# Kernel optimization log

Measured on AMD Instinct MI355X. Metric: run time of the kernel, lower is better.

Reference implementation:

```python
import jax, jax.numpy as jnp
import numpy as np

N, E, H, L, G = 80000, 1280000, 64, 4, 256
ATOM_V, ATOM_F, BOND_V, BOND_F = 100, 9, 10, 3
EPS = 1e-7

def _ln(x, g, b):
    mu = jnp.mean(x, axis=-1, keepdims=True)
    var = jnp.mean((x - mu) ** 2, axis=-1, keepdims=True)
    return (x - mu) * jax.lax.rsqrt(var + 1e-5) * g + b

def setup_inputs() -> dict:
    key = jax.random.key(0)
    ks = jax.random.split(key, 16)
    inp = {}
    inp['x'] = jax.random.randint(ks[0], (N, ATOM_F), 0, ATOM_V)
    inp['edge_attr'] = jax.random.randint(ks[1], (E, BOND_F), 0, BOND_V)
    inp['edge_index'] = jax.random.randint(ks[2], (2, E), 0, N)
    inp['batch'] = jnp.sort(jax.random.randint(ks[3], (N,), 0, G))
    s = 0.05
    inp['atom_emb'] = jax.random.normal(ks[4], (ATOM_F * ATOM_V, H)) * s
    inp['bond_emb'] = jax.random.normal(ks[5], (BOND_F * BOND_V, H)) * s
    inp['t'] = jnp.ones((L,))
    inp['W1'] = jax.random.normal(ks[6], (L, H, 2 * H)) * s
    inp['b1'] = jnp.zeros((L, 2 * H))
    inp['ln1_g'] = jnp.ones((L, 2 * H))
    inp['ln1_b'] = jnp.zeros((L, 2 * H))
    inp['W2'] = jax.random.normal(ks[7], (L, 2 * H, H)) * s
    inp['b2'] = jnp.zeros((L, H))
    inp['norm_g'] = jnp.ones((L, H))
    inp['norm_b'] = jnp.zeros((L, H))
    return inp

def reference(x, edge_attr, edge_index, batch, atom_emb, bond_emb, t,
              W1, b1, ln1_g, ln1_b, W2, b2, norm_g, norm_b):
    src, dst = edge_index[0], edge_index[1]
    # encoders: sum of per-feature embeddings (flattened tables with offsets)
    xn = jnp.sum(atom_emb[x + jnp.arange(ATOM_F) * ATOM_V], axis=1)   # [N,H]
    ea = jnp.sum(bond_emb[edge_attr + jnp.arange(BOND_F) * BOND_V], axis=1)  # [E,H]

    def genconv(h, l):
        msg = jax.nn.relu(h[src] + ea) + EPS                    # [E,H]
        m = msg * t[l]
        mx = jax.ops.segment_max(m, dst, num_segments=N)        # per-dst, per-channel
        ex = jnp.exp(m - mx[dst])
        den = jax.ops.segment_sum(ex, dst, num_segments=N)
        alpha = ex / (den[dst] + 1e-16)
        agg = jax.ops.segment_sum(alpha * msg, dst, num_segments=N)
        o = agg + h                                             # root add
        mid = jax.nn.relu(_ln(o @ W1[l] + b1[l], ln1_g[l], ln1_b[l]))
        return mid @ W2[l] + b2[l]

    cur = genconv(xn, 0)
    for l in range(1, L):  # res+ blocks: x + conv(act(norm(x)))  (dropout inactive in eval)
        hh = jax.nn.relu(_ln(cur, norm_g[l], norm_b[l]))
        cur = cur + genconv(hh, l)
    out = jax.nn.relu(_ln(cur, norm_g[0], norm_b[0]))
    # per-graph mean pooling
    sums = jax.ops.segment_sum(out, batch, num_segments=G)
    cnts = jax.ops.segment_sum(jnp.ones((out.shape[0],), out.dtype), batch, num_segments=G)
    return sums / jnp.maximum(cnts, 1.0)[:, None]
```

## Files before the change

### kernel.cpp

```cpp
#include <hip/hip_runtime.h>
#include <hip/hip_bf16.h>
#include <hip/hip_fp16.h>

#define NN 80000
#define NE 1280000
#define NL 4
#define NG 256

typedef __attribute__((ext_vector_type(8))) _Float16 half8;
typedef __attribute__((ext_vector_type(4))) float f32x4;

__device__ __forceinline__ float wave_sum(float v) {
    for (int off = 32; off; off >>= 1) v += __shfl_xor(v, off, 64);
    return v;
}

__global__ void k_count(const int* __restrict__ idx, int* __restrict__ cnt) {
    int e = blockIdx.x * 256 + threadIdx.x;
    if (e < NE) atomicAdd(&cnt[idx[e]], 1);
}

__global__ void k_scan1(const int* __restrict__ in, int* __restrict__ out,
                        int* __restrict__ bsum, int n) {
    __shared__ int ws[4];
    int i = blockIdx.x * 256 + threadIdx.x;
    int v = (i < n) ? in[i] : 0;
    int lane = threadIdx.x & 63, w = threadIdx.x >> 6;
    for (int off = 1; off < 64; off <<= 1) {
        int t = __shfl_up(v, off, 64);
        if (lane >= off) v += t;
    }
    if (lane == 63) ws[w] = v;
    __syncthreads();
    if (threadIdx.x == 0) {
        int acc = 0;
        for (int k = 0; k < 4; k++) { int t = ws[k]; ws[k] = acc; acc += t; }
    }
    __syncthreads();
    v += ws[w];
    if (i < n) out[i] = v;
    if (threadIdx.x == 255) bsum[blockIdx.x] = v;
}

__global__ void k_scan2(int* __restrict__ bsum, int nb) {
    __shared__ int ws[4];
    __shared__ int carry;
    if (threadIdx.x == 0) carry = 0;
    __syncthreads();
    for (int base = 0; base < nb; base += 256) {
        int i = base + threadIdx.x;
        int v = (i < nb) ? bsum[i] : 0;
        int lane = threadIdx.x & 63, w = threadIdx.x >> 6;
        for (int off = 1; off < 64; off <<= 1) {
            int t = __shfl_up(v, off, 64);
            if (lane >= off) v += t;
        }
        if (lane == 63) ws[w] = v;
        __syncthreads();
        if (threadIdx.x == 0) {
            int acc = carry;
            for (int k = 0; k < 4; k++) { int t = ws[k]; ws[k] = acc; acc += t; }
            carry = acc;
        }
        __syncthreads();
        v += ws[w];
        if (i < nb) bsum[i] = v;
        __syncthreads();
    }
}

__global__ void k_scan3(int* __restrict__ rowptr, const int* __restrict__ bsum, int n) {
    int i = blockIdx.x * 256 + threadIdx.x;
    if (i < n) {
        int off = (blockIdx.x > 0) ? bsum[blockIdx.x - 1] : 0;
        rowptr[1 + i] += off;
    }
    if (i == 0 && blockIdx.x == 0) rowptr[0] = 0;
}

__global__ void k_fill(const int* __restrict__ src, const int* __restrict__ dst,
                       const int* __restrict__ eattr, const int* __restrict__ rowptr,
                       int* __restrict__ wofs, int* __restrict__ csr32) {
    int part = blockIdx.x & 7;
    int e = (blockIdx.x >> 3) * 256 + threadIdx.x;
    if (e >= NE) return;
    int d = dst[e];
    if (d / 10000 != part) return;
    int pos = rowptr[d] + atomicAdd(&wofs[d], 1);
    int a0 = eattr[e * 3], a1 = eattr[e * 3 + 1], a2 = eattr[e * 3 + 2];
    csr32[pos] = (src[e] << 10) | (a0 + a1 * 10 + a2 * 100);
}

__global__ void k_prep(const float* __restrict__ bond_emb, __half* __restrict__ comb,
                       const float* __restrict__ W1, const float* __restrict__ W2,
                       __half* __restrict__ w1t, __half* __restrict__ w2t,
                       const int* __restrict__ batch, int* __restrict__ gstart) {
    int idx = blockIdx.x * 256 + threadIdx.x;
    if (idx < NN) {
        int b = batch[idx];
        if (idx == 0) {
            for (int g = 0; g <= b; ++g) gstart[g] = 0;
        } else {
            int pb = batch[idx - 1];
            for (int g = pb + 1; g <= b; ++g) gstart[g] = idx;
        }
        if (idx == NN - 1) {
            for (int g = b + 1; g <= NG; ++g) gstart[g] = NN;
        }
    }
    if (idx < 64000) {
        int wid = idx >> 6, lane = idx & 63;
        int a0 = wid % 10, a1 = (wid / 10) % 10, a2 = wid / 100;
        comb[wid * 64 + lane] = __float2half(bond_emb[a0 * 64 + lane] +
                                             bond_emb[(10 + a1) * 64 + lane] +
                                             bond_emb[(20 + a2) * 64 + lane]);
    }
    if (idx < NL * 8192) {
        int l = idx >> 13, r = idx & 8191;
        int n1 = r >> 6, k1 = r & 63;
        w1t[idx] = __float2half(W1[(l * 64 + k1) * 128 + n1]);
        int n2 = r >> 7, k2 = r & 127;
        w2t[idx] = __float2half(W2[(l * 128 + k2) * 64 + n2]);
    }
}

__global__ void k_atom(const int* __restrict__ x, const float* __restrict__ atom_emb,
                       __half* __restrict__ xn) {
    int wid = (blockIdx.x * 256 + threadIdx.x) >> 6;
    int lane = threadIdx.x & 63;
    if (wid >= NN) return;
    float acc = 0.f;
#pragma unroll
    for (int f = 0; f < 9; f++) {
        int idx = x[wid * 9 + f] + f * 100;
        acc += atom_emb[idx * 64 + lane];
    }
    xn[wid * 64 + lane] = __float2half(acc);
}

__global__ __launch_bounds__(256) void k_agg3(
    const __half* __restrict__ hin, const int* __restrict__ rowptr,
    const int* __restrict__ csr32, const __half* __restrict__ comb,
    const float* __restrict__ t, int l, __half* __restrict__ o) {
    int w = blockIdx.x * 4 + (threadIdx.x >> 6);
    int lane = threadIdx.x & 63;
    int half = lane >> 5, lc = lane & 31;
    int node = w * 2 + half;
    float tl = t[l];
    const __half2* hin2 = (const __half2*)hin;
    const __half2* comb2 = (const __half2*)comb;
    long oi2 = (long)node * 32 + lc;
    __half2 hr2 = hin2[oi2];
    int rs0 = rowptr[w * 2], mid = rowptr[w * 2 + 1], re1 = rowptr[w * 2 + 2];
    int base = half ? mid : rs0;
    int cnt = half ? (re1 - mid) : (mid - rs0);
    int cmax = max(mid - rs0, re1 - mid);
    float den0 = 0.f, den1 = 0.f, num0 = 0.f, num1 = 0.f;
#pragma unroll 4
    for (int i = 0; i < cmax; ++i) {
        bool valid = i < cnt;
        int v = csr32[valid ? base + i : 0];
        __half2 h2 = hin2[(long)(v >> 10) * 32 + lc];
        __half2 c2 = comb2[(v & 1023) * 32 + lc];
        __half2 s2 = __hadd2(h2, c2);
        float m0 = fmaxf(__low2float(s2), 0.f) + 1e-7f;
        float m1 = fmaxf(__high2float(s2), 0.f) + 1e-7f;
        float e0 = valid ? __expf(m0 * tl) : 0.f;
        float e1 = valid ? __expf(m1 * tl) : 0.f;
        den0 += e0; num0 = fmaf(e0, m0, num0);
        den1 += e1; num1 = fmaf(e1, m1, num1);
    }
    float r0 = num0 / (den0 + 1e-16f) + __low2float(hr2);
    float r1 = num1 / (den1 + 1e-16f) + __high2float(hr2);
    ((__half2*)o)[oi2] = __floats2half2_rn(r0, r1);
}

__global__ __launch_bounds__(256) void k_mlp(
    const __half* __restrict__ o, int l,
    const __half* __restrict__ w1t, const __half* __restrict__ w2t,
    const float* __restrict__ b1, const float* __restrict__ g1,
    const float* __restrict__ bb1, const float* __restrict__ b2,
    float* __restrict__ cur, int residual,
    __half* __restrict__ hh, const float* __restrict__ ng, const float* __restrict__ nbv) {
    __shared__ __half midL[4][16][136];
    int w = threadIdx.x >> 6, lane = threadIdx.x & 63;
    int node0 = blockIdx.x * 64 + w * 16;
    int lm = lane & 15, lh = lane >> 4;

    const __half* ob = o + (long)(node0 + lm) * 64 + lh * 8;
    half8 a0 = *(const half8*)(ob);
    half8 a1 = *(const half8*)(ob + 32);
    const __half* w1b = w1t + l * 8192 + lm * 64 + lh * 8;
    f32x4 acc[8];
#pragma unroll
    for (int nb = 0; nb < 8; ++nb) {
        f32x4 c = {0.f, 0.f, 0.f, 0.f};
        half8 b0 = *(const half8*)(w1b + nb * 1024);
        half8 bx = *(const half8*)(w1b + nb * 1024 + 32);
        c = __builtin_amdgcn_mfma_f32_16x16x32_f16(a0, b0, c, 0, 0, 0);
        c = __builtin_amdgcn_mfma_f32_16x16x32_f16(a1, bx, c, 0, 0, 0);
        acc[nb] = c;
    }

    float bv[8], gv[8], bbv[8];
#pragma unroll
    for (int nb = 0; nb < 8; ++nb) {
        int n = l * 128 + nb * 16 + lm;
        bv[nb] = b1[n]; gv[nb] = g1[n]; bbv[nb] = bb1[n];
    }
    float ps[4] = {0.f, 0.f, 0.f, 0.f};
#pragma unroll
    for (int nb = 0; nb < 8; ++nb)
#pragma unroll
        for (int r = 0; r < 4; ++r) { acc[nb][r] += bv[nb]; ps[r] += acc[nb][r]; }
#pragma unroll
    for (int r = 0; r < 4; ++r) {
        for (int off = 1; off < 16; off <<= 1) ps[r] += __shfl_xor(ps[r], off, 64);
        ps[r] *= (1.f / 128.f);
    }
    float pv[4] = {0.f, 0.f, 0.f, 0.f};
#pragma unroll
    for (int nb = 0; nb < 8; ++nb)
#pragma unroll
        for (int r = 0; r < 4; ++r) { float d = acc[nb][r] - ps[r]; pv[r] = fmaf(d, d, pv[r]); }
#pragma unroll
    for (int r = 0; r < 4; ++r) {
        for (int off = 1; off < 16; off <<= 1) pv[r] += __shfl_xor(pv[r], off, 64);
        pv[r] = rsqrtf(pv[r] * (1.f / 128.f) + 1e-5f);
    }
#pragma unroll
    for (int nb = 0; nb < 8; ++nb)
#pragma unroll
        for (int r = 0; r < 4; ++r) {
            float m = fmaxf((acc[nb][r] - ps[r]) * pv[r] * gv[nb] + bbv[nb], 0.f);
            midL[w][lh * 4 + r][nb * 16 + lm] = __float2half(m);
        }

    const __half* mrow = &midL[w][lm][lh * 8];
    const __half* w2b = w2t + l * 8192 + lm * 128 + lh * 8;
    f32x4 acc2[4];
#pragma unroll
    for (int nb = 0; nb < 4; ++nb) acc2[nb] = (f32x4){0.f, 0.f, 0.f, 0.f};
#pragma unroll
    for (int kb = 0; kb < 4; ++kb) {
        half8 a = *(const half8*)(mrow + kb * 32);
#pragma unroll
        for (int nb = 0; nb < 4; ++nb) {
            half8 b = *(const half8*)(w2b + nb * 2048 + kb * 32);
            acc2[nb] = __builtin_amdgcn_mfma_f32_16x16x32_f16(a, b, acc2[nb], 0, 0, 0);
        }
    }

    float b2v[4], cps[4] = {0.f, 0.f, 0.f, 0.f};
    float cv[4][4];
#pragma unroll
    for (int nb = 0; nb < 4; ++nb) b2v[nb] = b2[l * 64 + nb * 16 + lm];
#pragma unroll
    for (int nb = 0; nb < 4; ++nb)
#pragma unroll
        for (int r = 0; r < 4; ++r) {
            long ci = (long)(node0 + lh * 4 + r) * 64 + nb * 16 + lm;
            float z = acc2[nb][r] + b2v[nb] + (residual ? cur[ci] : 0.f);
            cur[ci] = z;
            cv[nb][r] = z;
            cps[r] += z;
        }
    if (hh) {
        float gn[4], bn[4], mu[4], rv[4];
        float pvv[4] = {0.f, 0.f, 0.f, 0.f};
#pragma unroll
        for (int nb = 0; nb < 4; ++nb) { gn[nb] = ng[nb * 16 + lm]; bn[nb] = nbv[nb * 16 + lm]; }
#pragma unroll
        for (int r = 0; r < 4; ++r) {
            float s = cps[r];
            for (int off = 1; off < 16; off <<= 1) s += __shfl_xor(s, off, 64);
            mu[r] = s * (1.f / 64.f);
        }
#pragma unroll
        for (int nb = 0; nb < 4; ++nb)
#pragma unroll
            for (int r = 0; r < 4; ++r) { float d = cv[nb][r] - mu[r]; pvv[r] = fmaf(d, d, pvv[r]); }
#pragma unroll
        for (int r = 0; r < 4; ++r) {
            float s = pvv[r];
            for (int off = 1; off < 16; off <<= 1) s += __shfl_xor(s, off, 64);
            rv[r] = rsqrtf(s * (1.f / 64.f) + 1e-5f);
        }
#pragma unroll
        for (int nb = 0; nb < 4; ++nb)
#pragma unroll
            for (int r = 0; r < 4; ++r) {
                long ci = (long)(node0 + lh * 4 + r) * 64 + nb * 16 + lm;
                hh[ci] = __float2half(fmaxf((cv[nb][r] - mu[r]) * rv[r] * gn[nb] + bn[nb], 0.f));
            }
    }
}

__global__ __launch_bounds__(1024) void k_pool2(
    const float* __restrict__ cur, const int* __restrict__ gstart,
    const float* __restrict__ g, const float* __restrict__ b,
    float* __restrict__ out) {
    int gi = blockIdx.x;
    int lane = threadIdx.x & 63, w = threadIdx.x >> 6;
    int s = gstart[gi], e = gstart[gi + 1];
    float gg = g[lane], bb = b[lane];
    float acc = 0.f;
    for (int n = s + w; n < e; n += 16) {
        float v = cur[(long)n * 64 + lane];
        float mu = wave_sum(v) * (1.f / 64.f);
        float d = v - mu;
        float var = wave_sum(d * d) * (1.f / 64.f);
        acc += fmaxf(d * rsqrtf(var + 1e-5f) * gg + bb, 0.f);
    }
    __shared__ float sh[16][64];
    sh[w][lane] = acc;
    __syncthreads();
    if (w == 0) {
        float tot = 0.f;
#pragma unroll
        for (int k = 0; k < 16; ++k) tot += sh[k][lane];
        out[gi * 64 + lane] = tot / fmaxf((float)(e - s), 1.f);
    }
}

extern "C" void kernel_launch(void* const* d_in, const int* in_sizes, int n_in,
                              void* d_out, int out_size, void* d_ws, size_t ws_size,
                              hipStream_t stream) {
    (void)in_sizes; (void)n_in; (void)out_size; (void)ws_size;
    const int* x         = (const int*)d_in[0];
    const int* edge_attr = (const int*)d_in[1];
    const int* src       = (const int*)d_in[2];
    const int* dst       = src + NE;
    const int* batch     = (const int*)d_in[3];
    const float* atom_emb = (const float*)d_in[4];
    const float* bond_emb = (const float*)d_in[5];
    const float* t        = (const float*)d_in[6];
    const float* W1       = (const float*)d_in[7];
    const float* b1       = (const float*)d_in[8];
    const float* g1       = (const float*)d_in[9];
    const float* bb1      = (const float*)d_in[10];
    const float* W2       = (const float*)d_in[11];
    const float* b2       = (const float*)d_in[12];
    const float* norm_g   = (const float*)d_in[13];
    const float* norm_b   = (const float*)d_in[14];
    float* out = (float*)d_out;

    size_t off = 0;
    auto alloc = [&](size_t bytes) {
        void* p = (char*)d_ws + off;
        off += (bytes + 255) & ~(size_t)255;
        return p;
    };
    int*    count  = (int*)alloc((size_t)NN * 4);
    int*    wofs   = (int*)alloc((size_t)NN * 4);
    int*    rowptr = (int*)alloc((size_t)(NN + 1) * 4);
    int*    bsum   = (int*)alloc(4096);
    int*    csr32  = (int*)alloc((size_t)NE * 4);
    __half* comb   = (__half*)alloc(1000 * 64 * 2);
    __half* xnH    = (__half*)alloc((size_t)NN * 64 * 2);
    __half* hhH    = (__half*)alloc((size_t)NN * 64 * 2);
    __half* oH     = (__half*)alloc((size_t)NN * 64 * 2);
    float*  cur    = (float*)alloc((size_t)NN * 64 * 4);
    int*    gstart = (int*)alloc((size_t)(NG + 1) * 4);
    __half* w1t    = (__half*)alloc((size_t)NL * 8192 * 2);
    __half* w2t    = (__half*)alloc((size_t)NL * 8192 * 2);

    hipMemsetAsync(count, 0, (size_t)NN * 4, stream);
    hipMemsetAsync(wofs, 0, (size_t)NN * 4, stream);

    const int EB = (NE + 255) / 256;
    const int SB = (NN + 255) / 256;
    const int WB = (NN * 64 + 255) / 256;

    k_count<<<EB, 256, 0, stream>>>(dst, count);
    k_scan1<<<SB, 256, 0, stream>>>(count, rowptr + 1, bsum, NN);
    k_scan2<<<1, 256, 0, stream>>>(bsum, SB);
    k_scan3<<<SB, 256, 0, stream>>>(rowptr, bsum, NN);
    k_fill<<<EB * 8, 256, 0, stream>>>(src, dst, edge_attr, rowptr, wofs, csr32);
    k_prep<<<SB, 256, 0, stream>>>(bond_emb, comb, W1, W2, w1t, w2t, batch, gstart);
    k_atom<<<WB, 256, 0, stream>>>(x, atom_emb, xnH);

    const int AB = NN / 8;
    const int MBK = NN / 64;
    for (int l = 0; l < NL; ++l) {
        const __half* hin = (l == 0) ? xnH : hhH;
        __half* hh_out = (l < NL - 1) ? hhH : nullptr;
        const float* ngp = norm_g + (l + 1 < NL ? (l + 1) * 64 : 0);
        const float* nbp = norm_b + (l + 1 < NL ? (l + 1) * 64 : 0);
        k_agg3<<<AB, 256, 0, stream>>>(hin, rowptr, csr32, comb, t, l, oH);
        k_mlp<<<MBK, 256, 0, stream>>>(oH, l, w1t, w2t, b1, g1, bb1, b2,
                                       cur, l > 0, hh_out, ngp, nbp);
    }
    k_pool2<<<NG, 1024, 0, stream>>>(cur, gstart, norm_g, norm_b, out);
}
```

Measured before the change: 476.5 us.

## Fuse edge aggregation and node MLP into one per-layer kernel

Merges the softmax aggregation kernel and the MLP kernel into a single k_conv kernel. Each block of four waves aggregates 16 nodes into a shared-memory tile, then wave 0 runs the MFMA MLP on that tile. This removes the global o buffer round trip and one launch per layer. Because the fused kernel now reads hin from a neighbour and writes hh for the next layer, the two node buffers are ping-ponged. In exchange, three of four waves sit idle during the MLP phase, and each block does far less MLP work than before.

Result: slower. 520.8 us (+9.3%).

```diff
diff --git a/kernel.cpp b/kernel.cpp
--- a/kernel.cpp
+++ b/kernel.cpp
@@ -138,56 +138,59 @@
     xn[wid * 64 + lane] = __float2half(acc);
 }
 
-__global__ __launch_bounds__(256) void k_agg3(
+__global__ __launch_bounds__(256) void k_conv(
     const __half* __restrict__ hin, const int* __restrict__ rowptr,
     const int* __restrict__ csr32, const __half* __restrict__ comb,
-    const float* __restrict__ t, int l, __half* __restrict__ o) {
-    int w = blockIdx.x * 4 + (threadIdx.x >> 6);
-    int lane = threadIdx.x & 63;
-    int half = lane >> 5, lc = lane & 31;
-    int node = w * 2 + half;
-    float tl = t[l];
-    const __half2* hin2 = (const __half2*)hin;
-    const __half2* comb2 = (const __half2*)comb;
-    long oi2 = (long)node * 32 + lc;
-    __half2 hr2 = hin2[oi2];
-    int rs0 = rowptr[w * 2], mid = rowptr[w * 2 + 1], re1 = rowptr[w * 2 + 2];
-    int base = half ? mid : rs0;
-    int cnt = half ? (re1 - mid) : (mid - rs0);
-    int cmax = max(mid - rs0, re1 - mid);
-    float den0 = 0.f, den1 = 0.f, num0 = 0.f, num1 = 0.f;
-#pragma unroll 4
-    for (int i = 0; i < cmax; ++i) {
-        bool valid = i < cnt;
-        int v = csr32[valid ? base + i : 0];
-        __half2 h2 = hin2[(long)(v >> 10) * 32 + lc];
-        __half2 c2 = comb2[(v & 1023) * 32 + lc];
-        __half2 s2 = __hadd2(h2, c2);
-        float m0 = fmaxf(__low2float(s2), 0.f) + 1e-7f;
-        float m1 = fmaxf(__high2float(s2), 0.f) + 1e-7f;
-        float e0 = valid ? __expf(m0 * tl) : 0.f;
-        float e1 = valid ? __expf(m1 * tl) : 0.f;
-        den0 += e0; num0 = fmaf(e0, m0, num0);
-        den1 += e1; num1 = fmaf(e1, m1, num1);
-    }
-    float r0 = num0 / (den0 + 1e-16f) + __low2float(hr2);
-    float r1 = num1 / (den1 + 1e-16f) + __high2float(hr2);
-    ((__half2*)o)[oi2] = __floats2half2_rn(r0, r1);
-}
-
-__global__ __launch_bounds__(256) void k_mlp(
-    const __half* __restrict__ o, int l,
+    const float* __restrict__ t, int l,
     const __half* __restrict__ w1t, const __half* __restrict__ w2t,
     const float* __restrict__ b1, const float* __restrict__ g1,
     const float* __restrict__ bb1, const float* __restrict__ b2,
     float* __restrict__ cur, int residual,
     __half* __restrict__ hh, const float* __restrict__ ng, const float* __restrict__ nbv) {
-    __shared__ __half midL[4][16][136];
+    __shared__ __half o_tile[16][136];
+    __shared__ __half midL[16][136];
     int w = threadIdx.x >> 6, lane = threadIdx.x & 63;
-    int node0 = blockIdx.x * 64 + w * 16;
+    int node0 = blockIdx.x * 16;
+    int half = lane >> 5, lc = lane & 31;
+    float tl = t[l];
+    const __half2* hin2 = (const __half2*)hin;
+    const __half2* comb2 = (const __half2*)comb;
+
+#pragma unroll
+    for (int pass = 0; pass < 2; ++pass) {
+        int nb0 = w * 4 + pass * 2;
+        int ni = nb0 + half;
+        int node = node0 + ni;
+        __half2 hr2 = hin2[(long)node * 32 + lc];
+        int rs0 = rowptr[node0 + nb0], mid = rowptr[node0 + nb0 + 1],
+            re1 = rowptr[node0 + nb0 + 2];
+        int base = half ? mid : rs0;
+        int cnt = half ? (re1 - mid) : (mid - rs0);
+        int cmax = max(mid - rs0, re1 - mid);
+        float den0 = 0.f, den1 = 0.f, num0 = 0.f, num1 = 0.f;
+#pragma unroll 4
+        for (int i = 0; i < cmax; ++i) {
+            bool valid = i < cnt;
+            int v = csr32[valid ? base + i : 0];
+            __half2 h2 = hin2[(long)(v >> 10) * 32 + lc];
+            __half2 c2 = comb2[(v & 1023) * 32 + lc];
+            __half2 s2 = __hadd2(h2, c2);
+            float m0 = fmaxf(__low2float(s2), 0.f) + 1e-7f;
+            float m1 = fmaxf(__high2float(s2), 0.f) + 1e-7f;
+            float e0 = valid ? __expf(m0 * tl) : 0.f;
+            float e1 = valid ? __expf(m1 * tl) : 0.f;
+            den0 += e0; num0 = fmaf(e0, m0, num0);
+            den1 += e1; num1 = fmaf(e1, m1, num1);
+        }
+        float r0 = num0 / (den0 + 1e-16f) + __low2float(hr2);
+        float r1 = num1 / (den1 + 1e-16f) + __high2float(hr2);
+        ((__half2*)&o_tile[ni][0])[lc] = __floats2half2_rn(r0, r1);
+    }
+    __syncthreads();
+    if (w != 0) return;
+
     int lm = lane & 15, lh = lane >> 4;
-
-    const __half* ob = o + (long)(node0 + lm) * 64 + lh * 8;
+    const __half* ob = &o_tile[lm][lh * 8];
     half8 a0 = *(const half8*)(ob);
     half8 a1 = *(const half8*)(ob + 32);
     const __half* w1b = w1t + l * 8192 + lm * 64 + lh * 8;
@@ -233,10 +236,10 @@
 #pragma unroll
         for (int r = 0; r < 4; ++r) {
             float m = fmaxf((acc[nb][r] - ps[r]) * pv[r] * gv[nb] + bbv[nb], 0.f);
-            midL[w][lh * 4 + r][nb * 16 + lm] = __float2half(m);
-        }
-
-    const __half* mrow = &midL[w][lm][lh * 8];
+            midL[lh * 4 + r][nb * 16 + lm] = __float2half(m);
+        }
+
+    const __half* mrow = &midL[lm][lh * 8];
     const __half* w2b = w2t + l * 8192 + lm * 128 + lh * 8;
     f32x4 acc2[4];
 #pragma unroll
@@ -359,7 +362,6 @@
     __half* comb   = (__half*)alloc(1000 * 64 * 2);
     __half* xnH    = (__half*)alloc((size_t)NN * 64 * 2);
     __half* hhH    = (__half*)alloc((size_t)NN * 64 * 2);
-    __half* oH     = (__half*)alloc((size_t)NN * 64 * 2);
     float*  cur    = (float*)alloc((size_t)NN * 64 * 4);
     int*    gstart = (int*)alloc((size_t)(NG + 1) * 4);
     __half* w1t    = (__half*)alloc((size_t)NL * 8192 * 2);
@@ -380,15 +382,15 @@
     k_prep<<<SB, 256, 0, stream>>>(bond_emb, comb, W1, W2, w1t, w2t, batch, gstart);
     k_atom<<<WB, 256, 0, stream>>>(x, atom_emb, xnH);
 
-    const int AB = NN / 8;
-    const int MBK = NN / 64;
+    __half* bufs[2] = {hhH, xnH};
+    const int CB = NN / 16;
     for (int l = 0; l < NL; ++l) {
-        const __half* hin = (l == 0) ? xnH : hhH;
-        __half* hh_out = (l < NL - 1) ? hhH : nullptr;
+        const __half* hin = (l == 0) ? xnH : bufs[(l & 1) ^ 1];
+        __half* hh_out = (l < NL - 1) ? bufs[l & 1] : nullptr;
         const float* ngp = norm_g + (l + 1 < NL ? (l + 1) * 64 : 0);
         const float* nbp = norm_b + (l + 1 < NL ? (l + 1) * 64 : 0);
-        k_agg3<<<AB, 256, 0, stream>>>(hin, rowptr, csr32, comb, t, l, oH);
-        k_mlp<<<MBK, 256, 0, stream>>>(oH, l, w1t, w2t, b1, g1, bb1, b2,
+        k_conv<<<CB, 256, 0, stream>>>(hin, rowptr, csr32, comb, t, l,
+                                       w1t, w2t, b1, g1, bb1, b2,
                                        cur, l > 0, hh_out, ngp, nbp);
     }
     k_pool2<<<NG, 1024, 0, stream>>>(cur, gstart, norm_g, norm_b, out);
```
